# Kernel tuning notes

Hardware: AMD Instinct MI355X
Metric: run time of the kernel (lower is better)

Reference implementation:

```python
import jax, jax.numpy as jnp
import numpy as np

N = 100000
K = 8
S = 2048
E = 131072


def setup_inputs() -> dict:
    key = jax.random.key(0)
    k1, k2, k3, k4, k5, k6, k7 = jax.random.split(key, 7)
    return {
        "beta": jax.random.normal(k1, (N,), dtype=jnp.float32),
        "a": jax.random.normal(k2, (1,), dtype=jnp.float32),
        "Zp": jax.random.normal(k3, (K, N), dtype=jnp.float32),
        "Gp": jax.random.normal(k4, (N, K), dtype=jnp.float32),
        "sample_idx": jax.random.randint(k5, (S,), 0, N),
        "sparse_i": jax.random.randint(k6, (E,), 0, N),
        "sparse_j": jax.random.randint(k7, (E,), 0, N),
    }


def reference(beta, a, Zp, Gp, sample_idx, sparse_i, sparse_j):
    # Z: softmax over archetype dim k (dim=0 of [k, N])
    Z = jax.nn.softmax(Zp, axis=0)          # [k, N]
    G = jax.nn.sigmoid(Gp)                  # [N, k]
    ZtG = Z.T * G                           # [N, k]
    C = ZtG / ZtG.sum(axis=0)               # [N, k], column-normalized
    sp_a = jax.nn.softplus(a)               # [1]

    Zs = Z[:, sample_idx]                   # [k, S]
    Cs = C[sample_idx, :]                   # [S, k]
    beta_s = beta[sample_idx]               # [S]

    # non-edge term: all-pairs distances within the sample
    bpair = beta_s[:, None] + beta_s[None, :]          # [S, S]
    M = (Zs @ Cs @ Zs).T                               # [S, k]
    diff = M[:, None, :] - M[None, :, :] + 1e-06       # [S, S, k]
    dist = jnp.sqrt(jnp.sum(diff ** 2, axis=-1))       # [S, S]
    mat = jnp.exp(bpair - sp_a * dist)                 # [S, S]
    mat_nd = mat - jnp.diag(jnp.diagonal(mat))
    e_vec = jnp.exp(jnp.ones((S,), dtype=mat.dtype))   # faithful to torch.exp(ones)
    z_pdist1 = 0.5 * (e_vec @ (mat_nd @ e_vec))        # scalar

    # edge term over sampled edges
    M2 = Zs @ Cs                                       # [k, k]
    beta_e = beta[sparse_i] + beta[sparse_j]           # [E]
    di = (M2 @ Z[:, sparse_i]).T                       # [E, k]
    dj = (M2 @ Z[:, sparse_j]).T                       # [E, k]
    dd = di - dj + 1e-06                               # [E, k]
    z_pdist2 = jnp.sum(beta_e - sp_a * jnp.sqrt(jnp.sum(dd ** 2, axis=-1)))

    return z_pdist2 - z_pdist1
```

## Files before the change

### kernel.cpp

```cpp
#include <hip/hip_runtime.h>
#include <hip/hip_bf16.h>

#define N_NODES 100000
#define S_SAMP  2048
#define E_EDGE  131072
#define NB      391
#define PB      512

#define SPA_OFF     0
#define CNT_U32     8
#define CS_PART_OFF 64
#define M2P_OFF     (64 + 3200)
#define PART_OFF    (M2P_OFF + 512)
#define BS_OFF      (PART_OFF + 512)
#define MS_OFF      (BS_OFF + 2048)
#define ZT_OFF      (MS_OFF + 16384)
#define VT_OFF      (ZT_OFF + 800000)

__global__ __launch_bounds__(256) void k1(const float* __restrict__ beta,
                                          const float* __restrict__ a,
                                          const float* __restrict__ Zp,
                                          const float* __restrict__ Gp,
                                          const int* __restrict__ sidx,
                                          float* __restrict__ W) {
    const int tid = threadIdx.x, bid = blockIdx.x;
    const int n = bid * 256 + tid;
    const int lane = tid & 63, wave = tid >> 6;
    __shared__ float sred[4][64];

    float part[8] = {0,0,0,0,0,0,0,0};
    if (n < N_NODES) {
        float zv[8]; float mx = -1e30f;
        #pragma unroll
        for (int k = 0; k < 8; ++k) {
            zv[k] = Zp[(size_t)k * N_NODES + n];
            mx = fmaxf(mx, zv[k]);
        }
        float den = 0.f;
        #pragma unroll
        for (int k = 0; k < 8; ++k) { zv[k] = __expf(zv[k] - mx); den += zv[k]; }
        float inv = 1.f / den;
        float4 g0 = *(const float4*)&Gp[(size_t)n * 8];
        float4 g1 = *(const float4*)&Gp[(size_t)n * 8 + 4];
        float g[8] = {g0.x,g0.y,g0.z,g0.w,g1.x,g1.y,g1.z,g1.w};
        float zt[8];
        #pragma unroll
        for (int k = 0; k < 8; ++k) {
            float z = zv[k] * inv;
            zt[k] = z;
            part[k] = z / (1.f + __expf(-g[k]));
        }
        *(float4*)&W[ZT_OFF + (size_t)n * 8]     = make_float4(zt[0],zt[1],zt[2],zt[3]);
        *(float4*)&W[ZT_OFF + (size_t)n * 8 + 4] = make_float4(zt[4],zt[5],zt[6],zt[7]);
    }
    #pragma unroll
    for (int k = 0; k < 8; ++k) {
        float x = part[k];
        #pragma unroll
        for (int off = 32; off; off >>= 1) x += __shfl_down(x, off, 64);
        if (lane == 0) sred[wave][k] = x;
    }
    __syncthreads();
    if (tid < 8)
        W[CS_PART_OFF + bid * 8 + tid] =
            sred[0][tid] + sred[1][tid] + sred[2][tid] + sred[3][tid];
    if (n == 0) {
        float av = a[0];
        W[SPA_OFF] = fmaxf(av, 0.f) + log1pf(__expf(-fabsf(av)));
        ((unsigned*)W)[CNT_U32] = 0u;
    }

    if (bid < 8) {
        int s = bid * 256 + tid;
        int idx = sidx[s];
        float zv[8]; float mx = -1e30f;
        #pragma unroll
        for (int k = 0; k < 8; ++k) {
            zv[k] = Zp[(size_t)k * N_NODES + idx];
            mx = fmaxf(mx, zv[k]);
        }
        float den = 0.f;
        #pragma unroll
        for (int k = 0; k < 8; ++k) { zv[k] = __expf(zv[k] - mx); den += zv[k]; }
        float inv = 1.f / den;
        float4 g0 = *(const float4*)&Gp[(size_t)idx * 8];
        float4 g1 = *(const float4*)&Gp[(size_t)idx * 8 + 4];
        float g[8] = {g0.x,g0.y,g0.z,g0.w,g1.x,g1.y,g1.z,g1.w};
        float z[8], w8[8];
        #pragma unroll
        for (int k = 0; k < 8; ++k) {
            z[k]  = zv[k] * inv;
            w8[k] = z[k] / (1.f + __expf(-g[k]));
        }
        W[BS_OFF + s] = beta[idx];

        __syncthreads();
        #pragma unroll
        for (int k = 0; k < 8; ++k) {
            #pragma unroll
            for (int j = 0; j < 8; ++j) {
                float x = z[k] * w8[j];
                #pragma unroll
                for (int off = 32; off; off >>= 1) x += __shfl_down(x, off, 64);
                if (lane == 0) sred[wave][k * 8 + j] = x;
            }
        }
        __syncthreads();
        if (tid < 64)
            W[M2P_OFF + bid * 64 + tid] =
                sred[0][tid] + sred[1][tid] + sred[2][tid] + sred[3][tid];
    }
}

__global__ __launch_bounds__(256) void k2(const int* __restrict__ sidx,
                                          float* __restrict__ W) {
    const int tid = threadIdx.x, bid = blockIdx.x;
    __shared__ float sflat[256];
    __shared__ float sinv8[8];
    __shared__ float sM2[64];

    {
        int k = tid & 7, g = tid >> 3;
        float s = 0.f;
        for (int b = g; b < NB; b += 32) s += W[CS_PART_OFF + b * 8 + k];
        sflat[tid] = s;
    }
    __syncthreads();
    if (tid < 8) {
        float s = 0.f;
        #pragma unroll
        for (int g = 0; g < 32; ++g) s += sflat[g * 8 + tid];
        sinv8[tid] = 1.f / s;
    }
    __syncthreads();
    if (tid < 64) {
        float m = 0.f;
        #pragma unroll
        for (int b = 0; b < 8; ++b) m += W[M2P_OFF + b * 64 + tid];
        sM2[tid] = m * sinv8[tid & 7];
    }
    __syncthreads();

    int n = bid * 256 + tid;
    if (n < N_NODES) {
        float4 z0 = *(const float4*)&W[ZT_OFF + (size_t)n * 8];
        float4 z1 = *(const float4*)&W[ZT_OFF + (size_t)n * 8 + 4];
        float z[8] = {z0.x,z0.y,z0.z,z0.w,z1.x,z1.y,z1.z,z1.w};
        float v[8];
        #pragma unroll
        for (int k = 0; k < 8; ++k) {
            float acc = 0.f;
            #pragma unroll
            for (int j = 0; j < 8; ++j) acc += sM2[k * 8 + j] * z[j];
            v[k] = acc;
        }
        *(float4*)&W[VT_OFF + (size_t)n * 8]     = make_float4(v[0],v[1],v[2],v[3]);
        *(float4*)&W[VT_OFF + (size_t)n * 8 + 4] = make_float4(v[4],v[5],v[6],v[7]);
    }
    if (bid < 8) {
        int s = bid * 256 + tid;
        int idx = sidx[s];
        float4 z0 = *(const float4*)&W[ZT_OFF + (size_t)idx * 8];
        float4 z1 = *(const float4*)&W[ZT_OFF + (size_t)idx * 8 + 4];
        float z[8] = {z0.x,z0.y,z0.z,z0.w,z1.x,z1.y,z1.z,z1.w};
        float v[8];
        #pragma unroll
        for (int k = 0; k < 8; ++k) {
            float acc = 0.f;
            #pragma unroll
            for (int j = 0; j < 8; ++j) acc += sM2[k * 8 + j] * z[j];
            v[k] = acc;
        }
        *(float4*)&W[MS_OFF + (size_t)s * 8]     = make_float4(v[0],v[1],v[2],v[3]);
        *(float4*)&W[MS_OFF + (size_t)s * 8 + 4] = make_float4(v[4],v[5],v[6],v[7]);
    }
}

__global__ __launch_bounds__(256) void k3(const float* __restrict__ beta,
                                          const int* __restrict__ si,
                                          const int* __restrict__ sj,
                                          float* __restrict__ out,
                                          float* __restrict__ W) {
    const int tid = threadIdx.x, bid = blockIdx.x;
    const int lane = tid & 63, wave = tid >> 6;
    const int gtid = bid * 256 + tid;
    const float spa = W[SPA_OFF];
    const float* Ms = W + MS_OFF;
    const float* Bs = W + BS_OFF;

    float accp = 0.f;
    #pragma unroll
    for (int r = 0; r < 4; ++r) {
        int srow = bid * 4 + r;
        float4 m0 = *(const float4*)&Ms[(size_t)srow * 8];
        float4 m1 = *(const float4*)&Ms[(size_t)srow * 8 + 4];
        float bsv = Bs[srow];
        for (int t = tid; t < S_SAMP; t += 256) {
            float4 a0 = *(const float4*)&Ms[(size_t)t * 8];
            float4 a1 = *(const float4*)&Ms[(size_t)t * 8 + 4];
            float d, ss;
            d = m0.x - a0.x + 1e-6f; ss  = d * d;
            d = m0.y - a0.y + 1e-6f; ss += d * d;
            d = m0.z - a0.z + 1e-6f; ss += d * d;
            d = m0.w - a0.w + 1e-6f; ss += d * d;
            d = m1.x - a1.x + 1e-6f; ss += d * d;
            d = m1.y - a1.y + 1e-6f; ss += d * d;
            d = m1.z - a1.z + 1e-6f; ss += d * d;
            d = m1.w - a1.w + 1e-6f; ss += d * d;
            float val = __expf(bsv + Bs[t] - spa * sqrtf(ss));
            if (t != srow) accp += val;
        }
    }
    float accs;
    {
        int i = si[gtid], j = sj[gtid];
        const float* vt = W + VT_OFF;
        float4 vi0 = *(const float4*)&vt[(size_t)i * 8];
        float4 vi1 = *(const float4*)&vt[(size_t)i * 8 + 4];
        float4 vj0 = *(const float4*)&vt[(size_t)j * 8];
        float4 vj1 = *(const float4*)&vt[(size_t)j * 8 + 4];
        float d, ss;
        d = vi0.x - vj0.x + 1e-6f; ss  = d * d;
        d = vi0.y - vj0.y + 1e-6f; ss += d * d;
        d = vi0.z - vj0.z + 1e-6f; ss += d * d;
        d = vi0.w - vj0.w + 1e-6f; ss += d * d;
        d = vi1.x - vj1.x + 1e-6f; ss += d * d;
        d = vi1.y - vj1.y + 1e-6f; ss += d * d;
        d = vi1.z - vj1.z + 1e-6f; ss += d * d;
        d = vi1.w - vj1.w + 1e-6f; ss += d * d;
        accs = beta[i] + beta[j] - spa * sqrtf(ss);
    }

    float part = accs - 0.5f * 7.38905609893065f * accp;
    __shared__ float sw[4];
    #pragma unroll
    for (int off = 32; off; off >>= 1) part += __shfl_down(part, off, 64);
    if (lane == 0) sw[wave] = part;
    __syncthreads();
    if (tid == 0) W[PART_OFF + bid] = sw[0] + sw[1] + sw[2] + sw[3];

    __shared__ int sLast;
    if (tid == 0) {
        __threadfence();
        unsigned old = atomicAdd(&((unsigned*)W)[CNT_U32], 1u);
        sLast = (old == PB - 1);
    }
    __syncthreads();
    if (sLast) {
        __threadfence();
        __shared__ double sd[256];
        double s = 0.0;
        for (int i = tid; i < PB; i += 256) s += (double)W[PART_OFF + i];
        sd[tid] = s;
        __syncthreads();
        for (int k = 128; k > 0; k >>= 1) {
            if (tid < k) sd[tid] += sd[tid + k];
            __syncthreads();
        }
        if (tid == 0) out[0] = (float)sd[0];
    }
}

extern "C" void kernel_launch(void* const* d_in, const int* in_sizes, int n_in,
                              void* d_out, int out_size, void* d_ws, size_t ws_size,
                              hipStream_t stream) {
    const float* beta       = (const float*)d_in[0];
    const float* a          = (const float*)d_in[1];
    const float* Zp         = (const float*)d_in[2];
    const float* Gp         = (const float*)d_in[3];
    const int*   sample_idx = (const int*)d_in[4];
    const int*   sparse_i   = (const int*)d_in[5];
    const int*   sparse_j   = (const int*)d_in[6];
    float* out = (float*)d_out;
    float* W   = (float*)d_ws;

    k1<<<dim3(NB), dim3(256), 0, stream>>>(beta, a, Zp, Gp, sample_idx, W);
    k2<<<dim3(NB), dim3(256), 0, stream>>>(sample_idx, W);
    k3<<<dim3(PB), dim3(256), 0, stream>>>(beta, sparse_i, sparse_j, out, W);
}
```

Baseline: 63.36 us.

## Fuse three kernels into one persistent kernel with software grid barriers

Merges the three launches into a single 512-block kernel that uses atomic-counter grid barriers between the normalisation, projection and reduction phases. Sample-node work moves onto otherwise idle tail blocks, and sample Z values stay in registers across phases. The pairwise loop is restructured so each loaded column is reused across four rows. This removes launch gaps, but it relies on all 512 blocks being co-resident (launch_bounds 256,4) and adds a memset launch and spin-wait overhead.

```diff
diff --git a/kernel.cpp b/kernel.cpp
--- a/kernel.cpp
+++ b/kernel.cpp
@@ -1,128 +1,140 @@
 #include <hip/hip_runtime.h>
-#include <hip/hip_bf16.h>
 
 #define N_NODES 100000
 #define S_SAMP  2048
 #define E_EDGE  131072
-#define NB      391
-#define PB      512
+#define NBLK    512
+#define SBLK0   391
 
 #define SPA_OFF     0
-#define CNT_U32     8
+#define CNT_OFF     8
 #define CS_PART_OFF 64
-#define M2P_OFF     (64 + 3200)
+#define M2P_OFF     (CS_PART_OFF + NBLK*8)
 #define PART_OFF    (M2P_OFF + 512)
-#define BS_OFF      (PART_OFF + 512)
-#define MS_OFF      (BS_OFF + 2048)
-#define ZT_OFF      (MS_OFF + 16384)
-#define VT_OFF      (ZT_OFF + 800000)
-
-__global__ __launch_bounds__(256) void k1(const float* __restrict__ beta,
-                                          const float* __restrict__ a,
-                                          const float* __restrict__ Zp,
-                                          const float* __restrict__ Gp,
-                                          const int* __restrict__ sidx,
-                                          float* __restrict__ W) {
-    const int tid = threadIdx.x, bid = blockIdx.x;
-    const int n = bid * 256 + tid;
-    const int lane = tid & 63, wave = tid >> 6;
-    __shared__ float sred[4][64];
-
-    float part[8] = {0,0,0,0,0,0,0,0};
-    if (n < N_NODES) {
-        float zv[8]; float mx = -1e30f;
+#define BS_OFF      (PART_OFF + NBLK)
+#define MS_OFF      (BS_OFF + S_SAMP)
+#define ZT_OFF      (MS_OFF + S_SAMP*8)
+#define VT_OFF      (ZT_OFF + N_NODES*8)
+
+__device__ __forceinline__ void gridbar(unsigned* cnt, unsigned target) {
+    __syncthreads();
+    if (threadIdx.x == 0) {
+        __threadfence();
+        __hip_atomic_fetch_add(cnt, 1u, __ATOMIC_RELEASE, __HIP_MEMORY_SCOPE_AGENT);
+        while (__hip_atomic_load(cnt, __ATOMIC_ACQUIRE, __HIP_MEMORY_SCOPE_AGENT) < target)
+            __builtin_amdgcn_s_sleep(2);
+    }
+    __syncthreads();
+}
+
+__global__ __launch_bounds__(256, 4) void k_all(
+    const float* __restrict__ beta, const float* __restrict__ a,
+    const float* __restrict__ Zp,   const float* __restrict__ Gp,
+    const int* __restrict__ sidx,   const int* __restrict__ si,
+    const int* __restrict__ sj,     float* __restrict__ out,
+    float* __restrict__ W)
+{
+    const int tid  = threadIdx.x, bid = blockIdx.x;
+    const int lane = tid & 63,    wave = tid >> 6;
+    unsigned* cnt = (unsigned*)W + CNT_OFF;
+
+    __shared__ float  sred[4][64];
+    __shared__ float  sflat[256];
+    __shared__ float  sinv8[8];
+    __shared__ float  sM2[64];
+    __shared__ double sd[256];
+    __shared__ int    sLast;
+
+    const bool isSamp = (bid >= SBLK0) && (bid < SBLK0 + 8);
+    float zs[8], ws8[8];
+
+    {
+        int n = bid * 256 + tid;
+        float part[8] = {0,0,0,0,0,0,0,0};
+        if (n < N_NODES) {
+            float zv[8]; float mx = -1e30f;
+            #pragma unroll
+            for (int k = 0; k < 8; ++k) {
+                zv[k] = Zp[(size_t)k * N_NODES + n];
+                mx = fmaxf(mx, zv[k]);
+            }
+            float den = 0.f;
+            #pragma unroll
+            for (int k = 0; k < 8; ++k) { zv[k] = __expf(zv[k] - mx); den += zv[k]; }
+            float inv = 1.f / den;
+            float4 g0 = *(const float4*)&Gp[(size_t)n * 8];
+            float4 g1 = *(const float4*)&Gp[(size_t)n * 8 + 4];
+            float g[8] = {g0.x,g0.y,g0.z,g0.w,g1.x,g1.y,g1.z,g1.w};
+            float zt[8];
+            #pragma unroll
+            for (int k = 0; k < 8; ++k) {
+                float z = zv[k] * inv;
+                zt[k] = z;
+                part[k] = z / (1.f + __expf(-g[k]));
+            }
+            *(float4*)&W[ZT_OFF + (size_t)n * 8]     = make_float4(zt[0],zt[1],zt[2],zt[3]);
+            *(float4*)&W[ZT_OFF + (size_t)n * 8 + 4] = make_float4(zt[4],zt[5],zt[6],zt[7]);
+        }
         #pragma unroll
         for (int k = 0; k < 8; ++k) {
-            zv[k] = Zp[(size_t)k * N_NODES + n];
-            mx = fmaxf(mx, zv[k]);
-        }
-        float den = 0.f;
-        #pragma unroll
-        for (int k = 0; k < 8; ++k) { zv[k] = __expf(zv[k] - mx); den += zv[k]; }
-        float inv = 1.f / den;
-        float4 g0 = *(const float4*)&Gp[(size_t)n * 8];
-        float4 g1 = *(const float4*)&Gp[(size_t)n * 8 + 4];
-        float g[8] = {g0.x,g0.y,g0.z,g0.w,g1.x,g1.y,g1.z,g1.w};
-        float zt[8];
-        #pragma unroll
-        for (int k = 0; k < 8; ++k) {
-            float z = zv[k] * inv;
-            zt[k] = z;
-            part[k] = z / (1.f + __expf(-g[k]));
-        }
-        *(float4*)&W[ZT_OFF + (size_t)n * 8]     = make_float4(zt[0],zt[1],zt[2],zt[3]);
-        *(float4*)&W[ZT_OFF + (size_t)n * 8 + 4] = make_float4(zt[4],zt[5],zt[6],zt[7]);
-    }
-    #pragma unroll
-    for (int k = 0; k < 8; ++k) {
-        float x = part[k];
-        #pragma unroll
-        for (int off = 32; off; off >>= 1) x += __shfl_down(x, off, 64);
-        if (lane == 0) sred[wave][k] = x;
-    }
-    __syncthreads();
-    if (tid < 8)
-        W[CS_PART_OFF + bid * 8 + tid] =
-            sred[0][tid] + sred[1][tid] + sred[2][tid] + sred[3][tid];
-    if (n == 0) {
-        float av = a[0];
-        W[SPA_OFF] = fmaxf(av, 0.f) + log1pf(__expf(-fabsf(av)));
-        ((unsigned*)W)[CNT_U32] = 0u;
-    }
-
-    if (bid < 8) {
-        int s = bid * 256 + tid;
-        int idx = sidx[s];
-        float zv[8]; float mx = -1e30f;
-        #pragma unroll
-        for (int k = 0; k < 8; ++k) {
-            zv[k] = Zp[(size_t)k * N_NODES + idx];
-            mx = fmaxf(mx, zv[k]);
-        }
-        float den = 0.f;
-        #pragma unroll
-        for (int k = 0; k < 8; ++k) { zv[k] = __expf(zv[k] - mx); den += zv[k]; }
-        float inv = 1.f / den;
-        float4 g0 = *(const float4*)&Gp[(size_t)idx * 8];
-        float4 g1 = *(const float4*)&Gp[(size_t)idx * 8 + 4];
-        float g[8] = {g0.x,g0.y,g0.z,g0.w,g1.x,g1.y,g1.z,g1.w};
-        float z[8], w8[8];
-        #pragma unroll
-        for (int k = 0; k < 8; ++k) {
-            z[k]  = zv[k] * inv;
-            w8[k] = z[k] / (1.f + __expf(-g[k]));
-        }
-        W[BS_OFF + s] = beta[idx];
-
+            float x = part[k];
+            #pragma unroll
+            for (int off = 32; off; off >>= 1) x += __shfl_down(x, off, 64);
+            if (lane == 0) sred[wave][k] = x;
+        }
         __syncthreads();
-        #pragma unroll
-        for (int k = 0; k < 8; ++k) {
-            #pragma unroll
-            for (int j = 0; j < 8; ++j) {
-                float x = z[k] * w8[j];
+        if (tid < 8)
+            W[CS_PART_OFF + bid * 8 + tid] =
+                sred[0][tid] + sred[1][tid] + sred[2][tid] + sred[3][tid];
+        if (bid == NBLK - 1 && tid == 0) {
+            float av = a[0];
+            W[SPA_OFF] = fmaxf(av, 0.f) + log1pf(__expf(-fabsf(av)));
+        }
+        if (isSamp) {
+            int s = (bid - SBLK0) * 256 + tid;
+            int idx = sidx[s];
+            float zv[8]; float mx = -1e30f;
+            #pragma unroll
+            for (int k = 0; k < 8; ++k) {
+                zv[k] = Zp[(size_t)k * N_NODES + idx];
+                mx = fmaxf(mx, zv[k]);
+            }
+            float den = 0.f;
+            #pragma unroll
+            for (int k = 0; k < 8; ++k) { zv[k] = __expf(zv[k] - mx); den += zv[k]; }
+            float inv = 1.f / den;
+            float4 g0 = *(const float4*)&Gp[(size_t)idx * 8];
+            float4 g1 = *(const float4*)&Gp[(size_t)idx * 8 + 4];
+            float g[8] = {g0.x,g0.y,g0.z,g0.w,g1.x,g1.y,g1.z,g1.w};
+            #pragma unroll
+            for (int k = 0; k < 8; ++k) {
+                zs[k]  = zv[k] * inv;
+                ws8[k] = zs[k] / (1.f + __expf(-g[k]));
+            }
+            W[BS_OFF + s] = beta[idx];
+            __syncthreads();
+            #pragma unroll
+            for (int k = 0; k < 8; ++k) {
                 #pragma unroll
-                for (int off = 32; off; off >>= 1) x += __shfl_down(x, off, 64);
-                if (lane == 0) sred[wave][k * 8 + j] = x;
-            }
-        }
-        __syncthreads();
-        if (tid < 64)
-            W[M2P_OFF + bid * 64 + tid] =
-                sred[0][tid] + sred[1][tid] + sred[2][tid] + sred[3][tid];
-    }
-}
-
-__global__ __launch_bounds__(256) void k2(const int* __restrict__ sidx,
-                                          float* __restrict__ W) {
-    const int tid = threadIdx.x, bid = blockIdx.x;
-    __shared__ float sflat[256];
-    __shared__ float sinv8[8];
-    __shared__ float sM2[64];
+                for (int j = 0; j < 8; ++j) {
+                    float x = zs[k] * ws8[j];
+                    #pragma unroll
+                    for (int off = 32; off; off >>= 1) x += __shfl_down(x, off, 64);
+                    if (lane == 0) sred[wave][k * 8 + j] = x;
+                }
+            }
+            __syncthreads();
+            if (tid < 64)
+                W[M2P_OFF + (bid - SBLK0) * 64 + tid] =
+                    sred[0][tid] + sred[1][tid] + sred[2][tid] + sred[3][tid];
+        }
+    }
+    gridbar(cnt, NBLK);
 
     {
         int k = tid & 7, g = tid >> 3;
         float s = 0.f;
-        for (int b = g; b < NB; b += 32) s += W[CS_PART_OFF + b * 8 + k];
+        for (int b = g; b < NBLK; b += 32) s += W[CS_PART_OFF + b * 8 + k];
         sflat[tid] = s;
     }
     __syncthreads();
@@ -140,117 +152,110 @@
         sM2[tid] = m * sinv8[tid & 7];
     }
     __syncthreads();
-
-    int n = bid * 256 + tid;
-    if (n < N_NODES) {
-        float4 z0 = *(const float4*)&W[ZT_OFF + (size_t)n * 8];
-        float4 z1 = *(const float4*)&W[ZT_OFF + (size_t)n * 8 + 4];
-        float z[8] = {z0.x,z0.y,z0.z,z0.w,z1.x,z1.y,z1.z,z1.w};
-        float v[8];
-        #pragma unroll
-        for (int k = 0; k < 8; ++k) {
-            float acc = 0.f;
-            #pragma unroll
-            for (int j = 0; j < 8; ++j) acc += sM2[k * 8 + j] * z[j];
-            v[k] = acc;
-        }
-        *(float4*)&W[VT_OFF + (size_t)n * 8]     = make_float4(v[0],v[1],v[2],v[3]);
-        *(float4*)&W[VT_OFF + (size_t)n * 8 + 4] = make_float4(v[4],v[5],v[6],v[7]);
-    }
-    if (bid < 8) {
-        int s = bid * 256 + tid;
-        int idx = sidx[s];
-        float4 z0 = *(const float4*)&W[ZT_OFF + (size_t)idx * 8];
-        float4 z1 = *(const float4*)&W[ZT_OFF + (size_t)idx * 8 + 4];
-        float z[8] = {z0.x,z0.y,z0.z,z0.w,z1.x,z1.y,z1.z,z1.w};
-        float v[8];
-        #pragma unroll
-        for (int k = 0; k < 8; ++k) {
-            float acc = 0.f;
-            #pragma unroll
-            for (int j = 0; j < 8; ++j) acc += sM2[k * 8 + j] * z[j];
-            v[k] = acc;
-        }
-        *(float4*)&W[MS_OFF + (size_t)s * 8]     = make_float4(v[0],v[1],v[2],v[3]);
-        *(float4*)&W[MS_OFF + (size_t)s * 8 + 4] = make_float4(v[4],v[5],v[6],v[7]);
-    }
-}
-
-__global__ __launch_bounds__(256) void k3(const float* __restrict__ beta,
-                                          const int* __restrict__ si,
-                                          const int* __restrict__ sj,
-                                          float* __restrict__ out,
-                                          float* __restrict__ W) {
-    const int tid = threadIdx.x, bid = blockIdx.x;
-    const int lane = tid & 63, wave = tid >> 6;
-    const int gtid = bid * 256 + tid;
-    const float spa = W[SPA_OFF];
-    const float* Ms = W + MS_OFF;
-    const float* Bs = W + BS_OFF;
-
-    float accp = 0.f;
-    #pragma unroll
-    for (int r = 0; r < 4; ++r) {
-        int srow = bid * 4 + r;
-        float4 m0 = *(const float4*)&Ms[(size_t)srow * 8];
-        float4 m1 = *(const float4*)&Ms[(size_t)srow * 8 + 4];
-        float bsv = Bs[srow];
-        for (int t = tid; t < S_SAMP; t += 256) {
+    {
+        int n = bid * 256 + tid;
+        if (n < N_NODES) {
+            float4 z0 = *(const float4*)&W[ZT_OFF + (size_t)n * 8];
+            float4 z1 = *(const float4*)&W[ZT_OFF + (size_t)n * 8 + 4];
+            float z[8] = {z0.x,z0.y,z0.z,z0.w,z1.x,z1.y,z1.z,z1.w};
+            float v[8];
+            #pragma unroll
+            for (int k = 0; k < 8; ++k) {
+                float acc = 0.f;
+                #pragma unroll
+                for (int j = 0; j < 8; ++j) acc += sM2[k * 8 + j] * z[j];
+                v[k] = acc;
+            }
+            *(float4*)&W[VT_OFF + (size_t)n * 8]     = make_float4(v[0],v[1],v[2],v[3]);
+            *(float4*)&W[VT_OFF + (size_t)n * 8 + 4] = make_float4(v[4],v[5],v[6],v[7]);
+        }
+        if (isSamp) {
+            int s = (bid - SBLK0) * 256 + tid;
+            float v[8];
+            #pragma unroll
+            for (int k = 0; k < 8; ++k) {
+                float acc = 0.f;
+                #pragma unroll
+                for (int j = 0; j < 8; ++j) acc += sM2[k * 8 + j] * zs[j];
+                v[k] = acc;
+            }
+            *(float4*)&W[MS_OFF + (size_t)s * 8]     = make_float4(v[0],v[1],v[2],v[3]);
+            *(float4*)&W[MS_OFF + (size_t)s * 8 + 4] = make_float4(v[4],v[5],v[6],v[7]);
+        }
+    }
+    gridbar(cnt, 2 * NBLK);
+
+    {
+        const float spa = W[SPA_OFF];
+        const float* Ms = W + MS_OFF;
+        const float* Bs = W + BS_OFF;
+        float4 r0[4], r1[4]; float bsv[4]; int srow0 = bid * 4;
+        #pragma unroll
+        for (int r = 0; r < 4; ++r) {
+            r0[r] = *(const float4*)&Ms[(size_t)(srow0 + r) * 8];
+            r1[r] = *(const float4*)&Ms[(size_t)(srow0 + r) * 8 + 4];
+            bsv[r] = Bs[srow0 + r];
+        }
+        float accp = 0.f;
+        #pragma unroll
+        for (int m = 0; m < 8; ++m) {
+            int t = tid + 256 * m;
             float4 a0 = *(const float4*)&Ms[(size_t)t * 8];
             float4 a1 = *(const float4*)&Ms[(size_t)t * 8 + 4];
+            float bt = Bs[t];
+            #pragma unroll
+            for (int r = 0; r < 4; ++r) {
+                float d, ss;
+                d = r0[r].x - a0.x + 1e-6f; ss  = d * d;
+                d = r0[r].y - a0.y + 1e-6f; ss += d * d;
+                d = r0[r].z - a0.z + 1e-6f; ss += d * d;
+                d = r0[r].w - a0.w + 1e-6f; ss += d * d;
+                d = r1[r].x - a1.x + 1e-6f; ss += d * d;
+                d = r1[r].y - a1.y + 1e-6f; ss += d * d;
+                d = r1[r].z - a1.z + 1e-6f; ss += d * d;
+                d = r1[r].w - a1.w + 1e-6f; ss += d * d;
+                float val = __expf(bsv[r] + bt - spa * sqrtf(ss));
+                if (t != srow0 + r) accp += val;
+            }
+        }
+        float accs;
+        {
+            int e = bid * 256 + tid;
+            int i = si[e], j = sj[e];
+            const float* vt = W + VT_OFF;
+            float4 vi0 = *(const float4*)&vt[(size_t)i * 8];
+            float4 vi1 = *(const float4*)&vt[(size_t)i * 8 + 4];
+            float4 vj0 = *(const float4*)&vt[(size_t)j * 8];
+            float4 vj1 = *(const float4*)&vt[(size_t)j * 8 + 4];
             float d, ss;
-            d = m0.x - a0.x + 1e-6f; ss  = d * d;
-            d = m0.y - a0.y + 1e-6f; ss += d * d;
-            d = m0.z - a0.z + 1e-6f; ss += d * d;
-            d = m0.w - a0.w + 1e-6f; ss += d * d;
-            d = m1.x - a1.x + 1e-6f; ss += d * d;
-            d = m1.y - a1.y + 1e-6f; ss += d * d;
-            d = m1.z - a1.z + 1e-6f; ss += d * d;
-            d = m1.w - a1.w + 1e-6f; ss += d * d;
-            float val = __expf(bsv + Bs[t] - spa * sqrtf(ss));
-            if (t != srow) accp += val;
-        }
-    }
-    float accs;
-    {
-        int i = si[gtid], j = sj[gtid];
-        const float* vt = W + VT_OFF;
-        float4 vi0 = *(const float4*)&vt[(size_t)i * 8];
-        float4 vi1 = *(const float4*)&vt[(size_t)i * 8 + 4];
-        float4 vj0 = *(const float4*)&vt[(size_t)j * 8];
-        float4 vj1 = *(const float4*)&vt[(size_t)j * 8 + 4];
-        float d, ss;
-        d = vi0.x - vj0.x + 1e-6f; ss  = d * d;
-        d = vi0.y - vj0.y + 1e-6f; ss += d * d;
-        d = vi0.z - vj0.z + 1e-6f; ss += d * d;
-        d = vi0.w - vj0.w + 1e-6f; ss += d * d;
-        d = vi1.x - vj1.x + 1e-6f; ss += d * d;
-        d = vi1.y - vj1.y + 1e-6f; ss += d * d;
-        d = vi1.z - vj1.z + 1e-6f; ss += d * d;
-        d = vi1.w - vj1.w + 1e-6f; ss += d * d;
-        accs = beta[i] + beta[j] - spa * sqrtf(ss);
-    }
-
-    float part = accs - 0.5f * 7.38905609893065f * accp;
-    __shared__ float sw[4];
-    #pragma unroll
-    for (int off = 32; off; off >>= 1) part += __shfl_down(part, off, 64);
-    if (lane == 0) sw[wave] = part;
-    __syncthreads();
-    if (tid == 0) W[PART_OFF + bid] = sw[0] + sw[1] + sw[2] + sw[3];
-
-    __shared__ int sLast;
+            d = vi0.x - vj0.x + 1e-6f; ss  = d * d;
+            d = vi0.y - vj0.y + 1e-6f; ss += d * d;
+            d = vi0.z - vj0.z + 1e-6f; ss += d * d;
+            d = vi0.w - vj0.w + 1e-6f; ss += d * d;
+            d = vi1.x - vj1.x + 1e-6f; ss += d * d;
+            d = vi1.y - vj1.y + 1e-6f; ss += d * d;
+            d = vi1.z - vj1.z + 1e-6f; ss += d * d;
+            d = vi1.w - vj1.w + 1e-6f; ss += d * d;
+            accs = beta[i] + beta[j] - spa * sqrtf(ss);
+        }
+        float part = accs - 0.5f * 7.38905609893065f * accp;
+        #pragma unroll
+        for (int off = 32; off; off >>= 1) part += __shfl_down(part, off, 64);
+        if (lane == 0) sflat[wave] = part;
+        __syncthreads();
+        if (tid == 0)
+            W[PART_OFF + bid] = sflat[0] + sflat[1] + sflat[2] + sflat[3];
+    }
+
     if (tid == 0) {
         __threadfence();
-        unsigned old = atomicAdd(&((unsigned*)W)[CNT_U32], 1u);
-        sLast = (old == PB - 1);
+        unsigned old = __hip_atomic_fetch_add(cnt, 1u, __ATOMIC_ACQ_REL,
+                                              __HIP_MEMORY_SCOPE_AGENT);
+        sLast = (old == 3u * NBLK - 1u);
     }
     __syncthreads();
     if (sLast) {
-        __threadfence();
-        __shared__ double sd[256];
-        double s = 0.0;
-        for (int i = tid; i < PB; i += 256) s += (double)W[PART_OFF + i];
+        double s = (double)W[PART_OFF + tid] + (double)W[PART_OFF + tid + 256];
         sd[tid] = s;
         __syncthreads();
         for (int k = 128; k > 0; k >>= 1) {
@@ -274,7 +279,8 @@
     float* out = (float*)d_out;
     float* W   = (float*)d_ws;
 
-    k1<<<dim3(NB), dim3(256), 0, stream>>>(beta, a, Zp, Gp, sample_idx, W);
-    k2<<<dim3(NB), dim3(256), 0, stream>>>(sample_idx, W);
-    k3<<<dim3(PB), dim3(256), 0, stream>>>(beta, sparse_i, sparse_j, out, W);
+    hipMemsetAsync((char*)d_ws + CNT_OFF * 4, 0, 4, stream);
+    k_all<<<dim3(NBLK), dim3(256), 0, stream>>>(beta, a, Zp, Gp,
+                                                sample_idx, sparse_i, sparse_j,
+                                                out, W);
 }
```

Result: slower. 202.3 us (+219.3%).

## Fuse projection and distance kernels, recomputing M2 projections on the fly

Applied to the files above, without the earlier changes.

Removes the separate k2 pass that projected all N nodes through M2 and stored VT and Ms. The fused kernel now reduces M2 itself, projects the sampled Z rows and the edge endpoint differences on the fly, and computes both distance terms in one launch. This drops one kernel launch and a full write and read of the projected N×8 array. In exchange, every one of the 512 blocks repeats the M2/column-sum reduction and does extra 8×8 matvecs per pair.

```diff
diff --git a/kernel.cpp b/kernel.cpp
--- a/kernel.cpp
+++ b/kernel.cpp
@@ -1,5 +1,4 @@
 #include <hip/hip_runtime.h>
-#include <hip/hip_bf16.h>
 
 #define N_NODES 100000
 #define S_SAMP  2048
@@ -8,14 +7,13 @@
 #define PB      512
 
 #define SPA_OFF     0
-#define CNT_U32     8
+#define CNT_OFF     8
 #define CS_PART_OFF 64
-#define M2P_OFF     (64 + 3200)
+#define M2P_OFF     (CS_PART_OFF + 3200)
 #define PART_OFF    (M2P_OFF + 512)
-#define BS_OFF      (PART_OFF + 512)
-#define MS_OFF      (BS_OFF + 2048)
-#define ZT_OFF      (MS_OFF + 16384)
-#define VT_OFF      (ZT_OFF + 800000)
+#define BS_OFF      (PART_OFF + PB)
+#define ZS_OFF      (BS_OFF + S_SAMP)
+#define ZT_OFF      (ZS_OFF + S_SAMP*8)
 
 __global__ __launch_bounds__(256) void k1(const float* __restrict__ beta,
                                           const float* __restrict__ a,
@@ -64,10 +62,10 @@
     if (tid < 8)
         W[CS_PART_OFF + bid * 8 + tid] =
             sred[0][tid] + sred[1][tid] + sred[2][tid] + sred[3][tid];
-    if (n == 0) {
+    if (bid == NB - 1 && tid == 0) {
         float av = a[0];
         W[SPA_OFF] = fmaxf(av, 0.f) + log1pf(__expf(-fabsf(av)));
-        ((unsigned*)W)[CNT_U32] = 0u;
+        ((unsigned*)W)[CNT_OFF] = 0u;
     }
 
     if (bid < 8) {
@@ -92,6 +90,8 @@
             z[k]  = zv[k] * inv;
             w8[k] = z[k] / (1.f + __expf(-g[k]));
         }
+        *(float4*)&W[ZS_OFF + (size_t)s * 8]     = make_float4(z[0],z[1],z[2],z[3]);
+        *(float4*)&W[ZS_OFF + (size_t)s * 8 + 4] = make_float4(z[4],z[5],z[6],z[7]);
         W[BS_OFF + s] = beta[idx];
 
         __syncthreads();
@@ -112,12 +112,18 @@
     }
 }
 
-__global__ __launch_bounds__(256) void k2(const int* __restrict__ sidx,
-                                          float* __restrict__ W) {
+__global__ __launch_bounds__(256, 2) void k2(const float* __restrict__ beta,
+                                             const int* __restrict__ si,
+                                             const int* __restrict__ sj,
+                                             float* __restrict__ out,
+                                             float* __restrict__ W) {
     const int tid = threadIdx.x, bid = blockIdx.x;
-    __shared__ float sflat[256];
-    __shared__ float sinv8[8];
-    __shared__ float sM2[64];
+    const int lane = tid & 63, wave = tid >> 6;
+    __shared__ float  sflat[256];
+    __shared__ float  sinv8[8];
+    __shared__ float  sM2[64];
+    __shared__ double sd[256];
+    __shared__ int    sLast;
 
     {
         int k = tid & 7, g = tid >> 3;
@@ -141,116 +147,95 @@
     }
     __syncthreads();
 
-    int n = bid * 256 + tid;
-    if (n < N_NODES) {
-        float4 z0 = *(const float4*)&W[ZT_OFF + (size_t)n * 8];
-        float4 z1 = *(const float4*)&W[ZT_OFF + (size_t)n * 8 + 4];
+    const float spa = W[SPA_OFF];
+
+    float mr[4][8]; float bsv[4];
+    const int srow0 = bid * 4;
+    #pragma unroll
+    for (int r = 0; r < 4; ++r) {
+        float4 z0 = *(const float4*)&W[ZS_OFF + (size_t)(srow0 + r) * 8];
+        float4 z1 = *(const float4*)&W[ZS_OFF + (size_t)(srow0 + r) * 8 + 4];
         float z[8] = {z0.x,z0.y,z0.z,z0.w,z1.x,z1.y,z1.z,z1.w};
-        float v[8];
         #pragma unroll
         for (int k = 0; k < 8; ++k) {
             float acc = 0.f;
             #pragma unroll
             for (int j = 0; j < 8; ++j) acc += sM2[k * 8 + j] * z[j];
-            v[k] = acc;
-        }
-        *(float4*)&W[VT_OFF + (size_t)n * 8]     = make_float4(v[0],v[1],v[2],v[3]);
-        *(float4*)&W[VT_OFF + (size_t)n * 8 + 4] = make_float4(v[4],v[5],v[6],v[7]);
-    }
-    if (bid < 8) {
-        int s = bid * 256 + tid;
-        int idx = sidx[s];
-        float4 z0 = *(const float4*)&W[ZT_OFF + (size_t)idx * 8];
-        float4 z1 = *(const float4*)&W[ZT_OFF + (size_t)idx * 8 + 4];
+            mr[r][k] = acc;
+        }
+        bsv[r] = W[BS_OFF + srow0 + r];
+    }
+    float accp = 0.f;
+    #pragma unroll
+    for (int m = 0; m < 8; ++m) {
+        int t = tid + 256 * m;
+        float4 z0 = *(const float4*)&W[ZS_OFF + (size_t)t * 8];
+        float4 z1 = *(const float4*)&W[ZS_OFF + (size_t)t * 8 + 4];
         float z[8] = {z0.x,z0.y,z0.z,z0.w,z1.x,z1.y,z1.z,z1.w};
-        float v[8];
+        float av[8];
         #pragma unroll
         for (int k = 0; k < 8; ++k) {
             float acc = 0.f;
             #pragma unroll
             for (int j = 0; j < 8; ++j) acc += sM2[k * 8 + j] * z[j];
-            v[k] = acc;
-        }
-        *(float4*)&W[MS_OFF + (size_t)s * 8]     = make_float4(v[0],v[1],v[2],v[3]);
-        *(float4*)&W[MS_OFF + (size_t)s * 8 + 4] = make_float4(v[4],v[5],v[6],v[7]);
-    }
-}
-
-__global__ __launch_bounds__(256) void k3(const float* __restrict__ beta,
-                                          const int* __restrict__ si,
-                                          const int* __restrict__ sj,
-                                          float* __restrict__ out,
-                                          float* __restrict__ W) {
-    const int tid = threadIdx.x, bid = blockIdx.x;
-    const int lane = tid & 63, wave = tid >> 6;
-    const int gtid = bid * 256 + tid;
-    const float spa = W[SPA_OFF];
-    const float* Ms = W + MS_OFF;
-    const float* Bs = W + BS_OFF;
-
-    float accp = 0.f;
-    #pragma unroll
-    for (int r = 0; r < 4; ++r) {
-        int srow = bid * 4 + r;
-        float4 m0 = *(const float4*)&Ms[(size_t)srow * 8];
-        float4 m1 = *(const float4*)&Ms[(size_t)srow * 8 + 4];
-        float bsv = Bs[srow];
-        for (int t = tid; t < S_SAMP; t += 256) {
-            float4 a0 = *(const float4*)&Ms[(size_t)t * 8];
-            float4 a1 = *(const float4*)&Ms[(size_t)t * 8 + 4];
+            av[k] = acc;
+        }
+        float bt = W[BS_OFF + t];
+        #pragma unroll
+        for (int r = 0; r < 4; ++r) {
             float d, ss;
-            d = m0.x - a0.x + 1e-6f; ss  = d * d;
-            d = m0.y - a0.y + 1e-6f; ss += d * d;
-            d = m0.z - a0.z + 1e-6f; ss += d * d;
-            d = m0.w - a0.w + 1e-6f; ss += d * d;
-            d = m1.x - a1.x + 1e-6f; ss += d * d;
-            d = m1.y - a1.y + 1e-6f; ss += d * d;
-            d = m1.z - a1.z + 1e-6f; ss += d * d;
-            d = m1.w - a1.w + 1e-6f; ss += d * d;
-            float val = __expf(bsv + Bs[t] - spa * sqrtf(ss));
-            if (t != srow) accp += val;
-        }
-    }
+            d = mr[r][0] - av[0] + 1e-6f; ss  = d * d;
+            d = mr[r][1] - av[1] + 1e-6f; ss += d * d;
+            d = mr[r][2] - av[2] + 1e-6f; ss += d * d;
+            d = mr[r][3] - av[3] + 1e-6f; ss += d * d;
+            d = mr[r][4] - av[4] + 1e-6f; ss += d * d;
+            d = mr[r][5] - av[5] + 1e-6f; ss += d * d;
+            d = mr[r][6] - av[6] + 1e-6f; ss += d * d;
+            d = mr[r][7] - av[7] + 1e-6f; ss += d * d;
+            float val = __expf(bsv[r] + bt - spa * sqrtf(ss));
+            if (t != srow0 + r) accp += val;
+        }
+    }
+
     float accs;
     {
-        int i = si[gtid], j = sj[gtid];
-        const float* vt = W + VT_OFF;
-        float4 vi0 = *(const float4*)&vt[(size_t)i * 8];
-        float4 vi1 = *(const float4*)&vt[(size_t)i * 8 + 4];
-        float4 vj0 = *(const float4*)&vt[(size_t)j * 8];
-        float4 vj1 = *(const float4*)&vt[(size_t)j * 8 + 4];
-        float d, ss;
-        d = vi0.x - vj0.x + 1e-6f; ss  = d * d;
-        d = vi0.y - vj0.y + 1e-6f; ss += d * d;
-        d = vi0.z - vj0.z + 1e-6f; ss += d * d;
-        d = vi0.w - vj0.w + 1e-6f; ss += d * d;
-        d = vi1.x - vj1.x + 1e-6f; ss += d * d;
-        d = vi1.y - vj1.y + 1e-6f; ss += d * d;
-        d = vi1.z - vj1.z + 1e-6f; ss += d * d;
-        d = vi1.w - vj1.w + 1e-6f; ss += d * d;
+        int e = bid * 256 + tid;
+        int i = si[e], j = sj[e];
+        const float* zt = W + ZT_OFF;
+        float4 i0 = *(const float4*)&zt[(size_t)i * 8];
+        float4 i1 = *(const float4*)&zt[(size_t)i * 8 + 4];
+        float4 j0 = *(const float4*)&zt[(size_t)j * 8];
+        float4 j1 = *(const float4*)&zt[(size_t)j * 8 + 4];
+        float dz[8] = {i0.x - j0.x, i0.y - j0.y, i0.z - j0.z, i0.w - j0.w,
+                       i1.x - j1.x, i1.y - j1.y, i1.z - j1.z, i1.w - j1.w};
+        float ss = 0.f;
+        #pragma unroll
+        for (int k = 0; k < 8; ++k) {
+            float acc = 0.f;
+            #pragma unroll
+            for (int jj = 0; jj < 8; ++jj) acc += sM2[k * 8 + jj] * dz[jj];
+            acc += 1e-6f;
+            ss += acc * acc;
+        }
         accs = beta[i] + beta[j] - spa * sqrtf(ss);
     }
 
     float part = accs - 0.5f * 7.38905609893065f * accp;
-    __shared__ float sw[4];
     #pragma unroll
     for (int off = 32; off; off >>= 1) part += __shfl_down(part, off, 64);
-    if (lane == 0) sw[wave] = part;
-    __syncthreads();
-    if (tid == 0) W[PART_OFF + bid] = sw[0] + sw[1] + sw[2] + sw[3];
-
-    __shared__ int sLast;
+    if (lane == 0) sflat[wave] = part;
+    __syncthreads();
+    if (tid == 0) W[PART_OFF + bid] = sflat[0] + sflat[1] + sflat[2] + sflat[3];
+
     if (tid == 0) {
         __threadfence();
-        unsigned old = atomicAdd(&((unsigned*)W)[CNT_U32], 1u);
+        unsigned old = atomicAdd(&((unsigned*)W)[CNT_OFF], 1u);
         sLast = (old == PB - 1);
     }
     __syncthreads();
     if (sLast) {
         __threadfence();
-        __shared__ double sd[256];
-        double s = 0.0;
-        for (int i = tid; i < PB; i += 256) s += (double)W[PART_OFF + i];
+        double s = (double)W[PART_OFF + tid] + (double)W[PART_OFF + tid + 256];
         sd[tid] = s;
         __syncthreads();
         for (int k = 128; k > 0; k >>= 1) {
@@ -275,6 +260,5 @@
     float* W   = (float*)d_ws;
 
     k1<<<dim3(NB), dim3(256), 0, stream>>>(beta, a, Zp, Gp, sample_idx, W);
-    k2<<<dim3(NB), dim3(256), 0, stream>>>(sample_idx, W);
-    k3<<<dim3(PB), dim3(256), 0, stream>>>(beta, sparse_i, sparse_j, out, W);
+    k2<<<dim3(PB), dim3(256), 0, stream>>>(beta, sparse_i, sparse_j, out, W);
 }
```

Result: faster. 57.94 us (-8.6%).
